# Performance work log

Hardware: AMD Instinct MI355X
Metric: run time of the kernel (lower is better)

## Reference

```python
import jax, jax.numpy as jnp
import numpy as np

B, T, D, H = 2, 2048, 1024, 16
HD = D // H  # 64
SCALE = 1.0 / np.sqrt(D).astype(np.float32)  # module uses 1/sqrt(mod_dim), not head_dim


def setup_inputs() -> dict:
    key = jax.random.key(0)
    k1, k2, k3 = jax.random.split(key, 3)
    x = jax.random.normal(k1, (B, T, D), dtype=jnp.float32)
    W_attn = jax.random.normal(k2, (3 * D, D), dtype=jnp.float32) * 0.02
    W_out = jax.random.normal(k3, (D, D), dtype=jnp.float32) * 0.02
    return {"x": x, "W_attn": W_attn, "W_out": W_out}


def reference(x, W_attn, W_out):
    b, t, d = x.shape
    # qkv projection (Linear, no bias): x @ W^T
    qkv = jnp.einsum('btd,ed->bte', x, W_attn)  # [b, t, 3d]
    q, k, v = jnp.split(qkv, 3, axis=-1)
    # [b, h, t, hd]
    q = q.reshape(b, t, H, HD).transpose(0, 2, 1, 3)
    k = k.reshape(b, t, H, HD).transpose(0, 2, 1, 3)
    v = v.reshape(b, t, H, HD).transpose(0, 2, 1, 3)
    # raw scores, causal mask applied before scaling (scale*-inf == -inf, so
    # equivalent to the original mask-then-scale order)
    att = jnp.einsum('bhqd,bhkd->bhqk', q, k)
    causal = jnp.tril(jnp.ones((t, t), dtype=bool))
    att = jnp.where(causal[None, None], att * SCALE, -jnp.inf)
    att = jax.nn.softmax(att, axis=-1)
    z = jnp.einsum('bhqk,bhkd->bhqd', att, v)
    z = z.transpose(0, 2, 1, 3).reshape(b, t, d)
    return jnp.einsum('btd,od->bto', z, W_out)
```

## Files before the change

### kernel.cpp

```cpp
#include <hip/hip_runtime.h>
#include <cstddef>

typedef unsigned short u16;
typedef __attribute__((ext_vector_type(4))) float floatx4;
typedef __attribute__((ext_vector_type(8))) short short8;

#define TT 2048
#define DD 1024
#define NH 16
#define ATT_SCALE (1.0f / 32.0f)
#define PSTR 72

__device__ __forceinline__ u16 f2bf(float f) {
  unsigned u = __builtin_bit_cast(unsigned, f);
  u += 0x7fffu + ((u >> 16) & 1u);
  return (u16)(u >> 16);
}

__device__ __forceinline__ unsigned pack2(float a, float b) {
#if __has_builtin(__builtin_amdgcn_cvt_pk_bf16_f32)
  auto t = __builtin_amdgcn_cvt_pk_bf16_f32(a, b);
  return __builtin_bit_cast(unsigned, t);
#else
  unsigned ua = __builtin_bit_cast(unsigned, a);
  ua += 0x7fffu + ((ua >> 16) & 1u);
  unsigned ub = __builtin_bit_cast(unsigned, b);
  ub += 0x7fffu + ((ub >> 16) & 1u);
  return (ua >> 16) | (ub & 0xffff0000u);
#endif
}

__device__ __forceinline__ void g2l16(const u16* g, u16* l) {
#if __has_builtin(__builtin_amdgcn_global_load_lds)
  __builtin_amdgcn_global_load_lds(
      (const __attribute__((address_space(1))) unsigned int*)g,
      (__attribute__((address_space(3))) unsigned int*)l, 16, 0, 0);
#else
  *(int4*)l = *(const int4*)g;
#endif
}

__device__ __forceinline__ short8 scale_q(short8 q) {
  short8 r;
#pragma unroll
  for (int i = 0; i < 8; ++i) {
    float f = __builtin_bit_cast(float, ((unsigned)(u16)q[i]) << 16) * ATT_SCALE;
    r[i] = (short)f2bf(f);
  }
  return r;
}

__global__ __launch_bounds__(256) void cvt3_kernel(const float* __restrict__ a,
                                                   const float* __restrict__ b,
                                                   const float* __restrict__ c,
                                                   u16* __restrict__ out,
                                                   int na, int nb, int nc) {
  int i = blockIdx.x * 256 + threadIdx.x;
  const float* src;
  int j;
  if (i < na) { src = a; j = i; }
  else if (i < na + nb) { src = b; j = i - na; }
  else if (i < na + nb + nc) { src = c; j = i - na - nb; }
  else return;
  float4 v = ((const float4*)src)[j];
  ((ushort4*)out)[i] = make_ushort4(f2bf(v.x), f2bf(v.y), f2bf(v.z), f2bf(v.w));
}

template <int MODE, int BN>
__global__ __launch_bounds__(256) void gemm_bt(const u16* __restrict__ A,
                                               const u16* __restrict__ Bm,
                                               void* __restrict__ C,
                                               u16* __restrict__ vt,
                                               int M, int N, int K) {
  constexpr int NT = BN / 32;
  __shared__ u16 As[128 * 32];
  __shared__ u16 Bs[BN * 32];
  const int tid = threadIdx.x;
  const int lane = tid & 63;
  const int wave = tid >> 6;
  const int quad = lane >> 4;
  const int l16 = lane & 15;
  const int wm = (wave >> 1) * 64;
  const int wn = (wave & 1) * (BN / 2);
  const int m0 = blockIdx.x * 128;
  const int n0 = blockIdx.y * BN;

  const int srow = wave * 16 + (lane >> 2);
  const int scol = (lane & 3) * 8;
  const int sl = wave * 512 + lane * 8;

  floatx4 acc[4][NT] = {};

  for (int k0 = 0; k0 < K; k0 += 32) {
    __syncthreads();
    g2l16(&A[(size_t)(m0 + srow) * K + k0 + scol], &As[sl]);
    g2l16(&A[(size_t)(m0 + 64 + srow) * K + k0 + scol], &As[2048 + sl]);
    g2l16(&Bm[(size_t)(n0 + srow) * K + k0 + scol], &Bs[sl]);
    if (BN == 128)
      g2l16(&Bm[(size_t)(n0 + 64 + srow) * K + k0 + scol], &Bs[2048 + sl]);
    __syncthreads();

    short8 af[4];
#pragma unroll
    for (int mt = 0; mt < 4; ++mt)
      af[mt] = *(const short8*)&As[(wm + mt * 16 + l16) * 32 + quad * 8];
#pragma unroll
    for (int nt = 0; nt < NT; ++nt) {
      short8 bf = *(const short8*)&Bs[(wn + nt * 16 + l16) * 32 + quad * 8];
#pragma unroll
      for (int mt = 0; mt < 4; ++mt)
        acc[mt][nt] = __builtin_amdgcn_mfma_f32_16x16x32_bf16(af[mt], bf, acc[mt][nt], 0, 0, 0);
    }
  }

  if (MODE == 2 && n0 >= 2048) {
    const int bidx = m0 >> 11;
    const int tbase = (m0 & 2047) + wm;
#pragma unroll
    for (int mt = 0; mt < 4; ++mt)
#pragma unroll
      for (int nt = 0; nt < NT; ++nt) {
        int gn = n0 + wn + nt * 16 + l16;
        size_t vrow = (size_t)(bidx * 1024 + gn - 2048);
        int t = tbase + mt * 16 + quad * 4;
        uint2 val;
        val.x = pack2(acc[mt][nt][0], acc[mt][nt][1]);
        val.y = pack2(acc[mt][nt][2], acc[mt][nt][3]);
        *(uint2*)&vt[vrow * TT + t] = val;
      }
  } else {
    const int cw = (MODE == 2) ? 2048 : N;
#pragma unroll
    for (int mt = 0; mt < 4; ++mt)
#pragma unroll
      for (int nt = 0; nt < NT; ++nt)
#pragma unroll
        for (int r = 0; r < 4; ++r) {
          int gm = m0 + wm + mt * 16 + quad * 4 + r;
          int gn = n0 + wn + nt * 16 + l16;
          float v = acc[mt][nt][r];
          if (MODE >= 1)
            ((u16*)C)[(size_t)gm * cw + gn] = f2bf(v);
          else
            ((float*)C)[(size_t)gm * cw + gn] = v;
        }
  }
}

__global__ __launch_bounds__(256) void attn_flash4(const u16* __restrict__ qk,
                                                   const u16* __restrict__ vt,
                                                   u16* __restrict__ z) {
  __shared__ u16 Ks[64 * PSTR];
  __shared__ u16 Vs[64 * PSTR];
  __shared__ u16 Ps[4][2][16 * PSTR];

  const int tid = threadIdx.x;
  const int lane = tid & 63;
  const int wave = tid >> 6;
  const int quad = lane >> 4;
  const int l16 = lane & 15;

  const int p = blockIdx.x;
  const int qtA = p, qtB = 31 - p;
  const int bh = blockIdx.y;
  const int b = bh >> 4, h = bh & 15;

  const size_t bbase = (size_t)b * TT * 2048;
  const u16* qg = qk + bbase + h * 64;
  const u16* kg = qk + bbase + 1024 + h * 64;
  const u16* vtg = vt + (size_t)bh * 64 * TT;

  short8 qfA[2], qfB[2];
  {
    const size_t ra = (size_t)(qtA * 64 + wave * 16 + l16) * 2048;
    const size_t rb = (size_t)(qtB * 64 + wave * 16 + l16) * 2048;
    qfA[0] = scale_q(*(const short8*)&qg[ra + quad * 8]);
    qfA[1] = scale_q(*(const short8*)&qg[ra + 32 + quad * 8]);
    qfB[0] = scale_q(*(const short8*)&qg[rb + quad * 8]);
    qfB[1] = scale_q(*(const short8*)&qg[rb + 32 + quad * 8]);
  }

  floatx4 OA[4] = {}, OB[4] = {};
  float psA = 0.f, psB = 0.f;

  const int str = tid >> 2, sc = (tid & 3) * 16;
  const int nktA = qtA + 1, nktB = qtB + 1;
  const int wl = wave * 16 + l16;

  for (int kt = 0; kt < nktB; ++kt) {
    const int kt0 = kt * 64;
    __syncthreads();
    *(int4*)&Ks[str * PSTR + sc] = *(const int4*)&kg[(size_t)(kt0 + str) * 2048 + sc];
    *(int4*)&Ks[str * PSTR + sc + 8] = *(const int4*)&kg[(size_t)(kt0 + str) * 2048 + sc + 8];
    *(int4*)&Vs[str * PSTR + sc] = *(const int4*)&vtg[(size_t)str * TT + kt0 + sc];
    *(int4*)&Vs[str * PSTR + sc + 8] = *(const int4*)&vtg[(size_t)str * TT + kt0 + sc + 8];
    __syncthreads();

    const bool actA = (kt < nktA);
    const bool diagA = (kt == qtA), diagB = (kt == qtB);

    floatx4 sB[4], sA[4];
#pragma unroll
    for (int nt = 0; nt < 4; ++nt) {
      short8 k0 = *(const short8*)&Ks[(nt * 16 + l16) * PSTR + quad * 8];
      short8 k1 = *(const short8*)&Ks[(nt * 16 + l16) * PSTR + 32 + quad * 8];
      floatx4 zz = {0.f, 0.f, 0.f, 0.f};
      sB[nt] = __builtin_amdgcn_mfma_f32_16x16x32_bf16(k0, qfB[0], zz, 0, 0, 0);
      sB[nt] = __builtin_amdgcn_mfma_f32_16x16x32_bf16(k1, qfB[1], sB[nt], 0, 0, 0);
      if (actA) {
        sA[nt] = __builtin_amdgcn_mfma_f32_16x16x32_bf16(k0, qfA[0], zz, 0, 0, 0);
        sA[nt] = __builtin_amdgcn_mfma_f32_16x16x32_bf16(k1, qfA[1], sA[nt], 0, 0, 0);
      }
    }

#pragma unroll
    for (int nt = 0; nt < 4; ++nt) {
      float e[4];
#pragma unroll
      for (int r = 0; r < 4; ++r) {
        int kl = nt * 16 + quad * 4 + r;
        e[r] = (!diagB || kl <= wl) ? __expf(sB[nt][r]) : 0.f;
        psB += e[r];
      }
      uint2 val = {pack2(e[0], e[1]), pack2(e[2], e[3])};
      *(uint2*)&Ps[wave][1][l16 * PSTR + nt * 16 + quad * 4] = val;
    }
    if (actA) {
#pragma unroll
      for (int nt = 0; nt < 4; ++nt) {
        float e[4];
#pragma unroll
        for (int r = 0; r < 4; ++r) {
          int kl = nt * 16 + quad * 4 + r;
          e[r] = (!diagA || kl <= wl) ? __expf(sA[nt][r]) : 0.f;
          psA += e[r];
        }
        uint2 val = {pack2(e[0], e[1]), pack2(e[2], e[3])};
        *(uint2*)&Ps[wave][0][l16 * PSTR + nt * 16 + quad * 4] = val;
      }
    }

    short8 pB0 = *(const short8*)&Ps[wave][1][l16 * PSTR + quad * 8];
    short8 pB1 = *(const short8*)&Ps[wave][1][l16 * PSTR + 32 + quad * 8];
    short8 pA0, pA1;
    if (actA) {
      pA0 = *(const short8*)&Ps[wave][0][l16 * PSTR + quad * 8];
      pA1 = *(const short8*)&Ps[wave][0][l16 * PSTR + 32 + quad * 8];
    }
#pragma unroll
    for (int nt = 0; nt < 4; ++nt) {
      short8 v0 = *(const short8*)&Vs[(nt * 16 + l16) * PSTR + quad * 8];
      short8 v1 = *(const short8*)&Vs[(nt * 16 + l16) * PSTR + 32 + quad * 8];
      OB[nt] = __builtin_amdgcn_mfma_f32_16x16x32_bf16(pB0, v0, OB[nt], 0, 0, 0);
      OB[nt] = __builtin_amdgcn_mfma_f32_16x16x32_bf16(pB1, v1, OB[nt], 0, 0, 0);
      if (actA) {
        OA[nt] = __builtin_amdgcn_mfma_f32_16x16x32_bf16(pA0, v0, OA[nt], 0, 0, 0);
        OA[nt] = __builtin_amdgcn_mfma_f32_16x16x32_bf16(pA1, v1, OA[nt], 0, 0, 0);
      }
    }
  }

  psA += __shfl_xor(psA, 16, 64);
  psA += __shfl_xor(psA, 32, 64);
  psB += __shfl_xor(psB, 16, 64);
  psB += __shfl_xor(psB, 32, 64);

#pragma unroll
  for (int r = 0; r < 4; ++r) {
    float rlA = 1.0f / __shfl(psA, quad * 4 + r, 64);
    float rlB = 1.0f / __shfl(psB, quad * 4 + r, 64);
    int qa = qtA * 64 + wave * 16 + quad * 4 + r;
    int qb = qtB * 64 + wave * 16 + quad * 4 + r;
#pragma unroll
    for (int nt = 0; nt < 4; ++nt) {
      int d = nt * 16 + l16;
      z[(size_t)(b * TT + qa) * DD + h * 64 + d] = f2bf(OA[nt][r] * rlA);
      z[(size_t)(b * TT + qb) * DD + h * 64 + d] = f2bf(OB[nt][r] * rlB);
    }
  }
}

extern "C" void kernel_launch(void* const* d_in, const int* in_sizes, int n_in,
                              void* d_out, int out_size, void* d_ws, size_t ws_size,
                              hipStream_t stream) {
  const float* x  = (const float*)d_in[0];
  const float* Wa = (const float*)d_in[1];
  const float* Wo = (const float*)d_in[2];
  float* out = (float*)d_out;

  u16* xb  = (u16*)d_ws;
  u16* Wab = xb  + (size_t)4096 * 1024;
  u16* Wob = Wab + (size_t)3072 * 1024;
  u16* qk  = Wob + (size_t)1024 * 1024;
  u16* z   = qk  + (size_t)4096 * 2048;
  u16* vt  = z   + (size_t)4096 * 1024;

  cvt3_kernel<<<8192, 256, 0, stream>>>(x, Wa, Wo, xb, 1048576, 786432, 262144);

  gemm_bt<2, 128><<<dim3(32, 24), 256, 0, stream>>>(xb, Wab, qk, vt, 4096, 3072, 1024);

  attn_flash4<<<dim3(16, 2 * NH), 256, 0, stream>>>(qk, vt, z);

  gemm_bt<0, 64><<<dim3(32, 16), 256, 0, stream>>>(z, Wob, out, nullptr, 4096, 1024, 1024);
}
```

Baseline: 195.5 us.

## Split attention KV loop across two wave groups with cross-group reduction

The attention kernel now launches 512 threads, and two groups of four waves process alternating key tiles, with double K/V shared buffers loaded together. At the end, the partial outputs and row sums are combined through shared memory. The P tile layout is also changed to a transposed scatter store with swapped MFMA operand order. This aims to double the waves per block so latency is hidden better, since the grid has only 512 blocks. The cost is extra shared memory, a final reduction step, and half the waves idling on odd tile counts.

```diff
diff --git a/kernel.cpp b/kernel.cpp
--- a/kernel.cpp
+++ b/kernel.cpp
@@ -147,16 +147,18 @@
   }
 }
 
-__global__ __launch_bounds__(256) void attn_flash4(const u16* __restrict__ qk,
+__global__ __launch_bounds__(512) void attn_flash5(const u16* __restrict__ qk,
                                                    const u16* __restrict__ vt,
                                                    u16* __restrict__ z) {
-  __shared__ u16 Ks[64 * PSTR];
-  __shared__ u16 Vs[64 * PSTR];
-  __shared__ u16 Ps[4][2][16 * PSTR];
+  __shared__ u16 Ks[2][64 * PSTR];
+  __shared__ u16 Vs[2][64 * PSTR];
+  __shared__ u16 Ps[8][16 * PSTR];
 
   const int tid = threadIdx.x;
   const int lane = tid & 63;
   const int wave = tid >> 6;
+  const int qs = wave & 3;
+  const int par = wave >> 2;
   const int quad = lane >> 4;
   const int l16 = lane & 15;
 
@@ -172,8 +174,8 @@
 
   short8 qfA[2], qfB[2];
   {
-    const size_t ra = (size_t)(qtA * 64 + wave * 16 + l16) * 2048;
-    const size_t rb = (size_t)(qtB * 64 + wave * 16 + l16) * 2048;
+    const size_t ra = (size_t)(qtA * 64 + qs * 16 + l16) * 2048;
+    const size_t rb = (size_t)(qtB * 64 + qs * 16 + l16) * 2048;
     qfA[0] = scale_q(*(const short8*)&qg[ra + quad * 8]);
     qfA[1] = scale_q(*(const short8*)&qg[ra + 32 + quad * 8]);
     qfB[0] = scale_q(*(const short8*)&qg[rb + quad * 8]);
@@ -181,101 +183,178 @@
   }
 
   floatx4 OA[4] = {}, OB[4] = {};
-  float psA = 0.f, psB = 0.f;
-
-  const int str = tid >> 2, sc = (tid & 3) * 16;
-  const int nktA = qtA + 1, nktB = qtB + 1;
-  const int wl = wave * 16 + l16;
-
-  for (int kt = 0; kt < nktB; ++kt) {
+  float psA[4] = {}, psB[4] = {};
+
+  const int tsel = tid >> 8;
+  const int t8 = tid & 255;
+  const int str = t8 >> 2, sc = (t8 & 3) * 16;
+
+  const int nktB = qtB + 1;
+  const int M = (nktB + 1) >> 1;
+  const int qrbA = qtA * 64 + qs * 16 + quad * 4;
+  const int qrbB = qtB * 64 + qs * 16 + quad * 4;
+
+  for (int m = 0; m < M; ++m) {
+    const int kt = 2 * m + par;
     const int kt0 = kt * 64;
     __syncthreads();
-    *(int4*)&Ks[str * PSTR + sc] = *(const int4*)&kg[(size_t)(kt0 + str) * 2048 + sc];
-    *(int4*)&Ks[str * PSTR + sc + 8] = *(const int4*)&kg[(size_t)(kt0 + str) * 2048 + sc + 8];
-    *(int4*)&Vs[str * PSTR + sc] = *(const int4*)&vtg[(size_t)str * TT + kt0 + sc];
-    *(int4*)&Vs[str * PSTR + sc + 8] = *(const int4*)&vtg[(size_t)str * TT + kt0 + sc + 8];
+    {
+      const int kst = 2 * m + tsel;
+      if (kst < nktB) {
+        *(int4*)&Ks[tsel][str * PSTR + sc] =
+            *(const int4*)&kg[(size_t)(kst * 64 + str) * 2048 + sc];
+        *(int4*)&Ks[tsel][str * PSTR + sc + 8] =
+            *(const int4*)&kg[(size_t)(kst * 64 + str) * 2048 + sc + 8];
+        *(int4*)&Vs[tsel][str * PSTR + sc] =
+            *(const int4*)&vtg[(size_t)str * TT + kst * 64 + sc];
+        *(int4*)&Vs[tsel][str * PSTR + sc + 8] =
+            *(const int4*)&vtg[(size_t)str * TT + kst * 64 + sc + 8];
+      }
+    }
     __syncthreads();
 
-    const bool actA = (kt < nktA);
-    const bool diagA = (kt == qtA), diagB = (kt == qtB);
-
-    floatx4 sB[4], sA[4];
-#pragma unroll
-    for (int nt = 0; nt < 4; ++nt) {
-      short8 k0 = *(const short8*)&Ks[(nt * 16 + l16) * PSTR + quad * 8];
-      short8 k1 = *(const short8*)&Ks[(nt * 16 + l16) * PSTR + 32 + quad * 8];
-      floatx4 zz = {0.f, 0.f, 0.f, 0.f};
-      sB[nt] = __builtin_amdgcn_mfma_f32_16x16x32_bf16(k0, qfB[0], zz, 0, 0, 0);
-      sB[nt] = __builtin_amdgcn_mfma_f32_16x16x32_bf16(k1, qfB[1], sB[nt], 0, 0, 0);
-      if (actA) {
-        sA[nt] = __builtin_amdgcn_mfma_f32_16x16x32_bf16(k0, qfA[0], zz, 0, 0, 0);
-        sA[nt] = __builtin_amdgcn_mfma_f32_16x16x32_bf16(k1, qfA[1], sA[nt], 0, 0, 0);
-      }
-    }
-
-#pragma unroll
-    for (int nt = 0; nt < 4; ++nt) {
-      float e[4];
-#pragma unroll
-      for (int r = 0; r < 4; ++r) {
-        int kl = nt * 16 + quad * 4 + r;
-        e[r] = (!diagB || kl <= wl) ? __expf(sB[nt][r]) : 0.f;
-        psB += e[r];
-      }
-      uint2 val = {pack2(e[0], e[1]), pack2(e[2], e[3])};
-      *(uint2*)&Ps[wave][1][l16 * PSTR + nt * 16 + quad * 4] = val;
-    }
-    if (actA) {
+    if (kt < nktB) {
+      floatx4 s[4];
 #pragma unroll
       for (int nt = 0; nt < 4; ++nt) {
-        float e[4];
-#pragma unroll
-        for (int r = 0; r < 4; ++r) {
-          int kl = nt * 16 + quad * 4 + r;
-          e[r] = (!diagA || kl <= wl) ? __expf(sA[nt][r]) : 0.f;
-          psA += e[r];
-        }
-        uint2 val = {pack2(e[0], e[1]), pack2(e[2], e[3])};
-        *(uint2*)&Ps[wave][0][l16 * PSTR + nt * 16 + quad * 4] = val;
-      }
-    }
-
-    short8 pB0 = *(const short8*)&Ps[wave][1][l16 * PSTR + quad * 8];
-    short8 pB1 = *(const short8*)&Ps[wave][1][l16 * PSTR + 32 + quad * 8];
-    short8 pA0, pA1;
-    if (actA) {
-      pA0 = *(const short8*)&Ps[wave][0][l16 * PSTR + quad * 8];
-      pA1 = *(const short8*)&Ps[wave][0][l16 * PSTR + 32 + quad * 8];
-    }
-#pragma unroll
-    for (int nt = 0; nt < 4; ++nt) {
-      short8 v0 = *(const short8*)&Vs[(nt * 16 + l16) * PSTR + quad * 8];
-      short8 v1 = *(const short8*)&Vs[(nt * 16 + l16) * PSTR + 32 + quad * 8];
-      OB[nt] = __builtin_amdgcn_mfma_f32_16x16x32_bf16(pB0, v0, OB[nt], 0, 0, 0);
-      OB[nt] = __builtin_amdgcn_mfma_f32_16x16x32_bf16(pB1, v1, OB[nt], 0, 0, 0);
-      if (actA) {
-        OA[nt] = __builtin_amdgcn_mfma_f32_16x16x32_bf16(pA0, v0, OA[nt], 0, 0, 0);
-        OA[nt] = __builtin_amdgcn_mfma_f32_16x16x32_bf16(pA1, v1, OA[nt], 0, 0, 0);
-      }
-    }
-  }
-
-  psA += __shfl_xor(psA, 16, 64);
-  psA += __shfl_xor(psA, 32, 64);
-  psB += __shfl_xor(psB, 16, 64);
-  psB += __shfl_xor(psB, 32, 64);
-
-#pragma unroll
-  for (int r = 0; r < 4; ++r) {
-    float rlA = 1.0f / __shfl(psA, quad * 4 + r, 64);
-    float rlB = 1.0f / __shfl(psB, quad * 4 + r, 64);
-    int qa = qtA * 64 + wave * 16 + quad * 4 + r;
-    int qb = qtB * 64 + wave * 16 + quad * 4 + r;
-#pragma unroll
-    for (int nt = 0; nt < 4; ++nt) {
-      int d = nt * 16 + l16;
-      z[(size_t)(b * TT + qa) * DD + h * 64 + d] = f2bf(OA[nt][r] * rlA);
-      z[(size_t)(b * TT + qb) * DD + h * 64 + d] = f2bf(OB[nt][r] * rlB);
+        short8 k0 = *(const short8*)&Ks[par][(nt * 16 + l16) * PSTR + quad * 8];
+        short8 k1 = *(const short8*)&Ks[par][(nt * 16 + l16) * PSTR + 32 + quad * 8];
+        floatx4 zz = {0.f, 0.f, 0.f, 0.f};
+        s[nt] = __builtin_amdgcn_mfma_f32_16x16x32_bf16(qfB[0], k0, zz, 0, 0, 0);
+        s[nt] = __builtin_amdgcn_mfma_f32_16x16x32_bf16(qfB[1], k1, s[nt], 0, 0, 0);
+      }
+      if (kt == qtB) {
+#pragma unroll
+        for (int nt = 0; nt < 4; ++nt)
+#pragma unroll
+          for (int r = 0; r < 4; ++r) {
+            int kk = kt0 + nt * 16 + l16;
+            float pv = (kk <= qrbB + r) ? __expf(s[nt][r]) : 0.f;
+            psB[r] += pv;
+            Ps[wave][(quad * 4 + r) * PSTR + nt * 16 + l16] = f2bf(pv);
+          }
+      } else {
+#pragma unroll
+        for (int nt = 0; nt < 4; ++nt)
+#pragma unroll
+          for (int r = 0; r < 4; ++r) {
+            float pv = __expf(s[nt][r]);
+            psB[r] += pv;
+            Ps[wave][(quad * 4 + r) * PSTR + nt * 16 + l16] = f2bf(pv);
+          }
+      }
+      {
+        short8 p0 = *(const short8*)&Ps[wave][l16 * PSTR + quad * 8];
+        short8 p1 = *(const short8*)&Ps[wave][l16 * PSTR + 32 + quad * 8];
+#pragma unroll
+        for (int nt = 0; nt < 4; ++nt) {
+          short8 v0 = *(const short8*)&Vs[par][(nt * 16 + l16) * PSTR + quad * 8];
+          short8 v1 = *(const short8*)&Vs[par][(nt * 16 + l16) * PSTR + 32 + quad * 8];
+          OB[nt] = __builtin_amdgcn_mfma_f32_16x16x32_bf16(p0, v0, OB[nt], 0, 0, 0);
+          OB[nt] = __builtin_amdgcn_mfma_f32_16x16x32_bf16(p1, v1, OB[nt], 0, 0, 0);
+        }
+      }
+
+      if (kt <= qtA) {
+#pragma unroll
+        for (int nt = 0; nt < 4; ++nt) {
+          short8 k0 = *(const short8*)&Ks[par][(nt * 16 + l16) * PSTR + quad * 8];
+          short8 k1 = *(const short8*)&Ks[par][(nt * 16 + l16) * PSTR + 32 + quad * 8];
+          floatx4 zz = {0.f, 0.f, 0.f, 0.f};
+          s[nt] = __builtin_amdgcn_mfma_f32_16x16x32_bf16(qfA[0], k0, zz, 0, 0, 0);
+          s[nt] = __builtin_amdgcn_mfma_f32_16x16x32_bf16(qfA[1], k1, s[nt], 0, 0, 0);
+        }
+        if (kt == qtA) {
+#pragma unroll
+          for (int nt = 0; nt < 4; ++nt)
+#pragma unroll
+            for (int r = 0; r < 4; ++r) {
+              int kk = kt0 + nt * 16 + l16;
+              float pv = (kk <= qrbA + r) ? __expf(s[nt][r]) : 0.f;
+              psA[r] += pv;
+              Ps[wave][(quad * 4 + r) * PSTR + nt * 16 + l16] = f2bf(pv);
+            }
+        } else {
+#pragma unroll
+          for (int nt = 0; nt < 4; ++nt)
+#pragma unroll
+            for (int r = 0; r < 4; ++r) {
+              float pv = __expf(s[nt][r]);
+              psA[r] += pv;
+              Ps[wave][(quad * 4 + r) * PSTR + nt * 16 + l16] = f2bf(pv);
+            }
+        }
+        short8 p0 = *(const short8*)&Ps[wave][l16 * PSTR + quad * 8];
+        short8 p1 = *(const short8*)&Ps[wave][l16 * PSTR + 32 + quad * 8];
+#pragma unroll
+        for (int nt = 0; nt < 4; ++nt) {
+          short8 v0 = *(const short8*)&Vs[par][(nt * 16 + l16) * PSTR + quad * 8];
+          short8 v1 = *(const short8*)&Vs[par][(nt * 16 + l16) * PSTR + 32 + quad * 8];
+          OA[nt] = __builtin_amdgcn_mfma_f32_16x16x32_bf16(p0, v0, OA[nt], 0, 0, 0);
+          OA[nt] = __builtin_amdgcn_mfma_f32_16x16x32_bf16(p1, v1, OA[nt], 0, 0, 0);
+        }
+      }
+    }
+  }
+
+#pragma unroll
+  for (int off = 1; off < 16; off <<= 1)
+#pragma unroll
+    for (int r = 0; r < 4; ++r) {
+      psA[r] += __shfl_xor(psA[r], off, 64);
+      psB[r] += __shfl_xor(psB[r], off, 64);
+    }
+
+  float* red = (float*)Ps;
+  float* lred = red + 4096;
+  __syncthreads();
+  if (par == 1) {
+#pragma unroll
+    for (int nt = 0; nt < 4; ++nt)
+#pragma unroll
+      for (int r = 0; r < 4; ++r)
+        red[(qs * 16 + quad * 4 + r) * 64 + nt * 16 + l16] = OA[nt][r];
+    if (l16 == 0)
+#pragma unroll
+      for (int r = 0; r < 4; ++r) lred[qs * 16 + quad * 4 + r] = psA[r];
+  }
+  __syncthreads();
+  if (par == 0) {
+#pragma unroll
+    for (int r = 0; r < 4; ++r) {
+      int row = qs * 16 + quad * 4 + r;
+      float rl = 1.0f / (psA[r] + lred[row]);
+      int qa = qtA * 64 + row;
+#pragma unroll
+      for (int nt = 0; nt < 4; ++nt) {
+        float o = OA[nt][r] + red[row * 64 + nt * 16 + l16];
+        z[(size_t)(b * TT + qa) * DD + h * 64 + nt * 16 + l16] = f2bf(o * rl);
+      }
+    }
+  }
+  __syncthreads();
+  if (par == 1) {
+#pragma unroll
+    for (int nt = 0; nt < 4; ++nt)
+#pragma unroll
+      for (int r = 0; r < 4; ++r)
+        red[(qs * 16 + quad * 4 + r) * 64 + nt * 16 + l16] = OB[nt][r];
+    if (l16 == 0)
+#pragma unroll
+      for (int r = 0; r < 4; ++r) lred[qs * 16 + quad * 4 + r] = psB[r];
+  }
+  __syncthreads();
+  if (par == 0) {
+#pragma unroll
+    for (int r = 0; r < 4; ++r) {
+      int row = qs * 16 + quad * 4 + r;
+      float rl = 1.0f / (psB[r] + lred[row]);
+      int qb = qtB * 64 + row;
+#pragma unroll
+      for (int nt = 0; nt < 4; ++nt) {
+        float o = OB[nt][r] + red[row * 64 + nt * 16 + l16];
+        z[(size_t)(b * TT + qb) * DD + h * 64 + nt * 16 + l16] = f2bf(o * rl);
+      }
     }
   }
 }
@@ -299,7 +378,7 @@
 
   gemm_bt<2, 128><<<dim3(32, 24), 256, 0, stream>>>(xb, Wab, qk, vt, 4096, 3072, 1024);
 
-  attn_flash4<<<dim3(16, 2 * NH), 256, 0, stream>>>(qk, vt, z);
+  attn_flash5<<<dim3(16, 2 * NH), 512, 0, stream>>>(qk, vt, z);
 
   gemm_bt<0, 64><<<dim3(32, 16), 256, 0, stream>>>(z, Wob, out, nullptr, 4096, 1024, 1024);
 }
```

Measured after the change: 179.3 us. 1.09x faster.
